# Optimization experiments

Hardware: AMD Instinct MI355X
Metric: run time of the kernel (lower is better)

## Reference

```python
import jax, jax.numpy as jnp
import numpy as np

ANCHOR_SIZES = (128.0, 256.0, 512.0)
ANCHOR_RATIOS = (0.5, 1.0, 2.0)
IOU_THR = 0.3


def _conv(x, w, b, pad):
    y = jax.lax.conv_general_dilated(
        x, w, window_strides=(1, 1), padding=[(pad, pad), (pad, pad)],
        dimension_numbers=("NCHW", "OIHW", "NCHW"))
    return y + b[None, :, None, None]


def _make_anchors(grid_h, grid_w, stride):
    # torchvision-style cell anchors (ratio-major over scales), rounded
    scales = jnp.asarray(ANCHOR_SIZES, jnp.float32)
    ratios = jnp.asarray(ANCHOR_RATIOS, jnp.float32)
    h_r = jnp.sqrt(ratios)
    w_r = 1.0 / h_r
    ws = (w_r[:, None] * scales[None, :]).reshape(-1)  # (A,)
    hs = (h_r[:, None] * scales[None, :]).reshape(-1)
    base = jnp.round(jnp.stack([-ws, -hs, ws, hs], axis=1) / 2.0)  # (A,4)
    sx = jnp.arange(grid_w, dtype=jnp.float32) * stride
    sy = jnp.arange(grid_h, dtype=jnp.float32) * stride
    yy, xx = jnp.meshgrid(sy, sx, indexing="ij")
    shifts = jnp.stack([xx, yy, xx, yy], axis=-1).reshape(-1, 4)  # (HW,4)
    return (shifts[:, None, :] + base[None, :, :]).reshape(-1, 4)  # (HW*A,4)


def _apply_box(anchors, deltas):
    w = anchors[:, 2] - anchors[:, 0]
    h = anchors[:, 3] - anchors[:, 1]
    cx = anchors[:, 0] + 0.5 * w
    cy = anchors[:, 1] + 0.5 * h
    pcx = deltas[:, 0] * w + cx
    pcy = deltas[:, 1] * h + cy
    pw = jnp.exp(deltas[:, 2]) * w
    ph = jnp.exp(deltas[:, 3]) * h
    return jnp.stack([pcx - 0.5 * pw, pcy - 0.5 * ph,
                      pcx + 0.5 * pw, pcy + 0.5 * ph], axis=1)


def _clip(boxes, img_h, img_w):
    x1 = jnp.clip(boxes[:, 0], 0.0, img_w)
    y1 = jnp.clip(boxes[:, 1], 0.0, img_h)
    x2 = jnp.clip(boxes[:, 2], 0.0, img_w)
    y2 = jnp.clip(boxes[:, 3], 0.0, img_h)
    return jnp.stack([x1, y1, x2, y2], axis=1)


def _nms_keep(boxes, scores, thr):
    # returns boolean keep mask in ORIGINAL box order (all idxs identical in
    # the source's batched_nms call, so this is plain NMS)
    n = boxes.shape[0]
    order = jnp.argsort(-scores)
    b = boxes[order]
    area = (b[:, 2] - b[:, 0]) * (b[:, 3] - b[:, 1])
    lt = jnp.maximum(b[:, None, :2], b[None, :, :2])
    rb = jnp.minimum(b[:, None, 2:], b[None, :, 2:])
    wh = jnp.clip(rb - lt, 0.0, None)
    inter = wh[..., 0] * wh[..., 1]
    iou = inter / (area[:, None] + area[None, :] - inter + 1e-9)  # (N,N)
    idx = jnp.arange(n)

    def body(i, keep):
        sup = (iou[i] > thr) & (idx > i)
        return jnp.where(keep[i], keep & ~sup, keep)

    keep_sorted = jax.lax.fori_loop(0, n, body, jnp.ones(n, bool))
    return jnp.zeros(n, bool).at[order].set(keep_sorted)


def setup_inputs() -> dict:
    key = jax.random.key(0)
    ks = jax.random.split(key, 7)
    C, H, W = 256, 32, 32
    A = len(ANCHOR_SIZES) * len(ANCHOR_RATIOS)  # 9
    return {
        "features": jax.random.normal(ks[0], (1, C, H, W), jnp.float32),
        "image_size": 512,
        "conv_w": jax.random.normal(ks[1], (512, C, 3, 3), jnp.float32) * 0.01,
        "conv_b": jnp.zeros((512,), jnp.float32),
        "cls_w": jax.random.normal(ks[2], (2 * A, 512, 1, 1), jnp.float32) * 0.01,
        "cls_b": jnp.zeros((2 * A,), jnp.float32),
        "bbox_w": jax.random.normal(ks[3], (4 * A, 512, 1, 1), jnp.float32) * 0.01,
        "bbox_b": jnp.zeros((4 * A,), jnp.float32),
    }


def reference(features, image_size, conv_w, conv_b, cls_w, cls_b, bbox_w, bbox_b):
    img_h = img_w = float(image_size)
    x = jax.nn.relu(_conv(features, conv_w, conv_b, pad=1))
    logits = _conv(x, cls_w, cls_b, pad=0)          # (1, 2A, H, W)
    bbox_pred = _conv(x, bbox_w, bbox_b, pad=0)     # (1, 4A, H, W)
    probs = jax.nn.sigmoid(logits)
    fg_scores = probs[:, 1::2, :, :].reshape(-1)    # same flatten order as torch
    grid_h, grid_w = features.shape[2], features.shape[3]
    stride = image_size // grid_h
    anchors = _make_anchors(grid_h, grid_w, float(stride))
    proposals = _apply_box(anchors, bbox_pred.reshape(-1, 4))
    proposals = _clip(proposals, img_h, img_w)
    keep = _nms_keep(proposals, fg_scores, IOU_THR)
    # fixed-shape output: suppressed boxes zeroed, plus the keep mask
    return proposals * keep[:, None].astype(proposals.dtype), probs, keep
```

## Files before the change

### kernel.cpp

```cpp
#include <hip/hip_runtime.h>
#include <math.h>

#define X_B      0
#define BBOX_B   2097152
#define PROPS_B  2244608
#define KEYS_B   2392064
#define RANK_B   2465792
#define SKEYS_B  2502656
#define SBOX_B   2576384
#define MASK_B   2725888
#define INTRA_B  KEYS_B
#define WS_NEED  13400000

typedef unsigned long long u64;
typedef double v4d __attribute__((ext_vector_type(4)));

__global__ __launch_bounds__(256, 2) void conv3x3_mfma_k(
    const float* __restrict__ feat, const float* __restrict__ w,
    const float* __restrict__ bias, float* __restrict__ xout)
{
  __shared__ float wl[9216];
  __shared__ float fl[8704];

  const int tid = threadIdx.x;
  const int ct = blockIdx.x >> 4;
  const int g  = blockIdx.x & 15;
  const int co0 = ct << 4;
  const int y0  = g << 1;

  for (int i = tid; i < 8704; i += 256) fl[i] = 0.0f;

  const int lane = tid & 63, wv = tid >> 6;
  const int q = lane >> 4, n = lane & 15;
  const int wy = wv >> 1, xb = (wv & 1) << 4;
  const int xn = xb + n;

  v4d ac0 = {0.0, 0.0, 0.0, 0.0}, ac1 = {0.0, 0.0, 0.0, 0.0};
  v4d ac2 = {0.0, 0.0, 0.0, 0.0}, ac3 = {0.0, 0.0, 0.0, 0.0};
  const float4* feat4 = (const float4*)feat;

  __syncthreads();

  for (int c = 0; c < 4; ++c) {
    const int cb = c << 6;
    #pragma unroll
    for (int i = 0; i < 9; ++i) {
      const int idx4 = tid + (i << 8);
      const int co = idx4 / 144;
      const int s4 = idx4 - co * 144;
      const float4 v =
          *(const float4*)(w + (co0 + co) * 2304 + c * 576 + (s4 << 2));
      #pragma unroll
      for (int e = 0; e < 4; ++e) {
        const int s = (s4 << 2) + e;
        const int ci = s / 9;
        const int tap = s - ci * 9;
        wl[(((tap << 6) + ci) << 4) + co] = ((const float*)&v)[e];
      }
    }
    #pragma unroll
    for (int i = 0; i < 8; ++i) {
      const int idx4 = tid + (i << 8);
      const int ci = idx4 >> 5;
      const int rr = (idx4 >> 3) & 3;
      const int x4 = idx4 & 7;
      const int grow = y0 - 1 + rr;
      if ((unsigned)grow < 32u) {
        const float4 v = feat4[((cb + ci) << 8) + (grow << 3) + x4];
        float* p = &fl[ci * 136 + rr * 34 + 1 + (x4 << 2)];
        p[0] = v.x; p[1] = v.y; p[2] = v.z; p[3] = v.w;
      }
    }
    __syncthreads();
    #pragma unroll
    for (int tap = 0; tap < 9; ++tap) {
      const int ky = tap / 3, kx = tap - 3 * (tap / 3);
      const float* ab = &wl[(tap << 10) + (q << 4) + n];
      const float* bb = &fl[q * 136 + (wy + ky) * 34 + xn + kx];
      #pragma unroll
      for (int u = 0; u < 16; u += 4) {
        ac0 = __builtin_amdgcn_mfma_f64_16x16x4f64(
            (double)ab[(u + 0) << 6], (double)bb[(u + 0) * 544], ac0, 0, 0, 0);
        ac1 = __builtin_amdgcn_mfma_f64_16x16x4f64(
            (double)ab[(u + 1) << 6], (double)bb[(u + 1) * 544], ac1, 0, 0, 0);
        ac2 = __builtin_amdgcn_mfma_f64_16x16x4f64(
            (double)ab[(u + 2) << 6], (double)bb[(u + 2) * 544], ac2, 0, 0, 0);
        ac3 = __builtin_amdgcn_mfma_f64_16x16x4f64(
            (double)ab[(u + 3) << 6], (double)bb[(u + 3) * 544], ac3, 0, 0, 0);
      }
    }
    __syncthreads();
  }

  const int pbase = (g << 6) + (wv << 4) + n;
  #pragma unroll
  for (int i = 0; i < 4; ++i) {
    const int co = co0 + q + (i << 2);
    const double s = (ac0[i] + ac1[i]) + (ac2[i] + ac3[i]);
    const double v = fmax(s + (double)bias[co], 0.0);
    xout[(co << 10) + pbase] = (float)v;
  }
}

#define CPITCH 38
#define CCHS   (18 * CPITCH)
__global__ __launch_bounds__(256) void conv3x3_relu_fb_k(
    const float* __restrict__ feat, const float* __restrict__ w,
    const float* __restrict__ bias, float* __restrict__ xout)
{
  __shared__ float il[2][8 * CCHS];
  const int cp = blockIdx.x >> 1, h = blockIdx.x & 1;
  const int tid = threadIdx.x;
  const int h16 = h << 4;
  const int co0 = cp << 1;
  for (int i = tid; i < 8 * CCHS; i += 256) { il[0][i] = 0.0f; il[1][i] = 0.0f; }
  const int yl = tid >> 4;
  const int x0 = (tid & 15) << 1;
  double aA0 = 0.0, aA1 = 0.0, aB0 = 0.0, aB1 = 0.0;
  const float4* feat4 = (const float4*)feat;
  float4 pf[5]; int pch[5], pt[5], pc4[5], pok[5];
  #pragma unroll
  for (int k = 0; k < 5; ++k) {
    const int i = tid + (k << 8);
    const int ch = i / 144, rem = i - ch * 144;
    const int t = rem >> 3, c4 = rem & 7;
    const int g = h16 - 1 + t;
    pch[k] = ch; pt[k] = t; pc4[k] = c4;
    pok[k] = (i < 1152) && ((unsigned)g < 32u);
    pf[k] = pok[k] ? feat4[(ch << 8) + (g << 3) + c4] : float4{0.f,0.f,0.f,0.f};
  }
  __syncthreads();
  for (int cc = 0; cc < 256; cc += 8) {
    const int buf = (cc >> 3) & 1;
    #pragma unroll
    for (int k = 0; k < 5; ++k)
      if (pok[k]) {
        float* p = &il[buf][pch[k] * CCHS + pt[k] * CPITCH + (pc4[k] << 2) + 1];
        p[0] = pf[k].x; p[1] = pf[k].y; p[2] = pf[k].z; p[3] = pf[k].w;
      }
    if (cc + 8 < 256) {
      #pragma unroll
      for (int k = 0; k < 5; ++k) {
        const int g = h16 - 1 + pt[k];
        if (pok[k]) pf[k] = feat4[((cc + 8 + pch[k]) << 8) + (g << 3) + pc4[k]];
      }
    }
    __syncthreads();
    #pragma unroll
    for (int cl = 0; cl < 8; ++cl) {
      const float* wAp = w + co0 * 2304 + (cc + cl) * 9;
      const float* wBp = wAp + 2304;
      double wa[9], wb[9];
      #pragma unroll
      for (int q = 0; q < 9; ++q) { wa[q] = (double)wAp[q]; wb[q] = (double)wBp[q]; }
      const float* ir = &il[buf][cl * CCHS + yl * CPITCH + x0];
      #pragma unroll
      for (int ky = 0; ky < 3; ++ky) {
        const float2 q0 = *(const float2*)(ir + ky * CPITCH);
        const float2 q1 = *(const float2*)(ir + ky * CPITCH + 2);
        const double v0 = (double)q0.x, v1 = (double)q0.y;
        const double v2 = (double)q1.x, v3 = (double)q1.y;
        aA0 += v0 * wa[3*ky+0] + v1 * wa[3*ky+1] + v2 * wa[3*ky+2];
        aA1 += v1 * wa[3*ky+0] + v2 * wa[3*ky+1] + v3 * wa[3*ky+2];
        aB0 += v0 * wb[3*ky+0] + v1 * wb[3*ky+1] + v2 * wb[3*ky+2];
        aB1 += v1 * wb[3*ky+0] + v2 * wb[3*ky+1] + v3 * wb[3*ky+2];
      }
    }
  }
  const double bA = (double)bias[co0], bB = (double)bias[co0 + 1];
  const int y = h16 + yl;
  float2 rA, rB;
  rA.x = (float)fmax(aA0 + bA, 0.0); rA.y = (float)fmax(aA1 + bA, 0.0);
  rB.x = (float)fmax(aB0 + bB, 0.0); rB.y = (float)fmax(aB1 + bB, 0.0);
  *(float2*)&xout[(co0 << 10) + (y << 5) + x0] = rA;
  *(float2*)&xout[((co0 + 1) << 10) + (y << 5) + x0] = rB;
}

__global__ __launch_bounds__(256) void head1x1_k(
    const float* __restrict__ x,
    const float* __restrict__ cls_w, const float* __restrict__ cls_b,
    const float* __restrict__ bbox_w, const float* __restrict__ bbox_b,
    float* __restrict__ out, float* __restrict__ bbox_out)
{
  __shared__ float wl[512];
  const int bid = blockIdx.x;
  const int co = bid >> 2;
  const int px = ((bid & 3) << 8) | threadIdx.x;
  const bool is_cls = co < 18;
  const float* wsrc = is_cls ? (cls_w + co * 512) : (bbox_w + (co - 18) * 512);
  for (int i = threadIdx.x; i < 512; i += 256) wl[i] = wsrc[i];
  __syncthreads();
  double acc0 = 0.0, acc1 = 0.0, acc2 = 0.0, acc3 = 0.0;
  #pragma unroll 4
  for (int c = 0; c < 512; c += 4) {
    acc0 += (double)x[((c + 0) << 10) | px] * (double)wl[c + 0];
    acc1 += (double)x[((c + 1) << 10) | px] * (double)wl[c + 1];
    acc2 += (double)x[((c + 2) << 10) | px] * (double)wl[c + 2];
    acc3 += (double)x[((c + 3) << 10) | px] * (double)wl[c + 3];
  }
  double acc = ((acc0 + acc1) + (acc2 + acc3)) +
               (double)(is_cls ? cls_b[co] : bbox_b[co - 18]);
  if (is_cls)
    out[36864 + (co << 10) + px] = (float)(1.0 / (1.0 + exp(-acc)));
  else
    bbox_out[((co - 18) << 10) + px] = (float)acc;
}

__global__ __launch_bounds__(256) void proposals_k(
    const float* __restrict__ bbox, const int* __restrict__ imgsz,
    const float* __restrict__ out, float* __restrict__ props,
    u64* __restrict__ keys, unsigned* __restrict__ rank)
{
  const int r = blockIdx.x * 256 + threadIdx.x;
  if (r >= 9216) return;
  const float4 d = ((const float4*)bbox)[r];
  const int cell = r / 9, a = r - cell * 9;
  const int ix = cell & 31, iy = cell >> 5;
  const int ri = a / 3, si = a - ri * 3;
  const double ratio = (ri == 0) ? 0.5 : (ri == 1 ? 1.0 : 2.0);
  const double scale = (si == 0) ? 128.0 : (si == 1 ? 256.0 : 512.0);
  const double hr = sqrt(ratio), wr = 1.0 / hr;
  const double bx = nearbyint(wr * scale * 0.5);
  const double by = nearbyint(hr * scale * 0.5);
  const double cx = ix * 16.0, cy = iy * 16.0;
  const double w = 2.0 * bx, hh = 2.0 * by;
  const double pcx = (double)d.x * w + cx;
  const double pcy = (double)d.y * hh + cy;
  const double pw = exp((double)d.z) * w;
  const double ph = exp((double)d.w) * hh;
  const double im = (double)imgsz[0];
  float4 o;
  o.x = (float)fmin(fmax(pcx - 0.5 * pw, 0.0), im);
  o.y = (float)fmin(fmax(pcy - 0.5 * ph, 0.0), im);
  o.z = (float)fmin(fmax(pcx + 0.5 * pw, 0.0), im);
  o.w = (float)fmin(fmax(pcy + 0.5 * ph, 0.0), im);
  ((float4*)props)[r] = o;
  const float s = out[36864 + ((2 * (r >> 10) + 1) << 10) + (r & 1023)];
  keys[r] = ((u64)__float_as_uint(s) << 32) | (unsigned)(0x7FFFFFFF - r);
  rank[r] = 0u;
}

__global__ __launch_bounds__(256) void rank_k(
    const u64* __restrict__ keys, unsigned* __restrict__ rank)
{
  const int jt = blockIdx.x % 36, ic = blockIdx.x / 36;
  const int j = jt * 256 + threadIdx.x;
  const u64 kj = keys[j];
  const int lane = threadIdx.x & 63;
  const int base = ic * 576;
  unsigned lo[9], hi[9];
  #pragma unroll
  for (int rr = 0; rr < 9; ++rr) {
    const u64 k = keys[base + rr * 64 + lane];
    lo[rr] = (unsigned)k; hi[rr] = (unsigned)(k >> 32);
  }
  unsigned cnt = 0;
  #pragma unroll
  for (int rr = 0; rr < 9; ++rr) {
    #pragma unroll
    for (int l = 0; l < 64; ++l) {
      const unsigned llo = (unsigned)__builtin_amdgcn_readlane((int)lo[rr], l);
      const unsigned lhi = (unsigned)__builtin_amdgcn_readlane((int)hi[rr], l);
      const u64 ki = ((u64)lhi << 32) | llo;
      cnt += (ki > kj) ? 1u : 0u;
    }
  }
  atomicAdd(&rank[j], cnt);
}

__global__ __launch_bounds__(256) void scatter_k(
    const u64* __restrict__ keys, const unsigned* __restrict__ rank,
    const float* __restrict__ props, u64* __restrict__ skeys,
    float4* __restrict__ sboxes)
{
  const int r = blockIdx.x * 256 + threadIdx.x;
  if (r >= 9216) return;
  const unsigned rk = rank[r];
  skeys[rk] = keys[r];
  sboxes[rk] = ((const float4*)props)[r];
}

__global__ __launch_bounds__(256) void mask_k(
    const float4* __restrict__ sb4, u64* __restrict__ mask,
    u64* __restrict__ intra)
{
  __shared__ __align__(16) float4 ib[64];
  const int ci = blockIdx.x;
  const int Wb = blockIdx.y << 2;
  const int i_lo = ci << 6;
  const int i_hi = min(i_lo + 64, (Wb + 4) << 6);
  if (i_lo >= i_hi) return;
  const int wv = threadIdx.x >> 6, lane = threadIdx.x & 63;
  const int W = Wb + wv;
  const int cnt = i_hi - i_lo;
  if (threadIdx.x < cnt) ib[threadIdx.x] = sb4[i_lo + threadIdx.x];
  __syncthreads();
  const float4 bj = sb4[(W << 6) + lane];
  const float areaJ = (bj.z - bj.x) * (bj.w - bj.y);
  const int wbase = W << 6;
  const int n = min(i_hi, wbase + 64) - i_lo;
  u64 intr = 0ULL;
  #pragma unroll 8
  for (int k = 0; k < n; ++k) {
    const float4 bi = ib[k];
    const float areaI = (bi.z - bi.x) * (bi.w - bi.y);
    const float ix1 = fmaxf(bj.x, bi.x), iy1 = fmaxf(bj.y, bi.y);
    const float ix2 = fminf(bj.z, bi.z), iy2 = fminf(bj.w, bi.w);
    const float iw = fmaxf(ix2 - ix1, 0.0f), ih = fmaxf(iy2 - iy1, 0.0f);
    const double inter = (double)iw * (double)ih;
    const double uni = (double)areaJ + (double)areaI - inter + 1e-9;
    const bool pred = inter > 0.3 * uni;
    const u64 bal = __ballot(pred);
    const int i = i_lo + k;
    if (lane == 0) mask[(size_t)i * 144 + W] = bal;
    if (i >= wbase) intr |= pred ? (1ULL << (i - wbase)) : 0ULL;
  }
  if (ci == W) intra[wbase + lane] = intr;
}

__global__ __launch_bounds__(1024) void sweep_out_k(
    const u64* __restrict__ mask, const u64* __restrict__ intra,
    const u64* __restrict__ skeys, const float4* __restrict__ sboxes,
    float* __restrict__ out)
{
  extern __shared__ __align__(16) char sm[];
  u64* subm   = (u64*)sm;
  u64* intraS = subm + 8192;
  u64* supS   = intraS + 1024;
  u64* keptS  = supS + 16;
  unsigned short* kpl = (unsigned short*)(keptS + 144);
  int* kcnt = (int*)(kpl + 9216);

  const int tid = threadIdx.x;
  const int lane = tid & 63, wv = tid >> 6;
  if (tid == 0) *kcnt = 0;
  if (tid < 144) keptS[tid] = 0ULL;
  if (tid < 16) supS[tid] = 0ULL;
  if (tid < 512) {
    const int wq = tid & 7, r0 = tid >> 3;
    #pragma unroll
    for (int k = 0; k < 8; ++k) {
      const int i = r0 + (k << 6);
      subm[i * 8 + wq] = mask[(size_t)i * 144 + wq];
    }
    if (wq == 0) intraS[r0] = intra[r0];
    if (wq == 1) intraS[64 + r0] = intra[64 + r0];
    if (wq == 2) intraS[128 + r0] = intra[128 + r0];
    if (wq == 3) intraS[192 + r0] = intra[192 + r0];
    if (wq == 4) intraS[256 + r0] = intra[256 + r0];
    if (wq == 5) intraS[320 + r0] = intra[320 + r0];
    if (wq == 6) intraS[384 + r0] = intra[384 + r0];
    if (wq == 7) intraS[448 + r0] = intra[448 + r0];
  }
  __syncthreads();

  for (int sg = 0; sg < 18; ++sg) {
    const int buf = sg & 1;
    const int wbase = sg << 3;
    const int ibase = wbase << 6;
    if (tid < 512) {
      const int K = *kcnt;
      const int wq = tid & 7;
      u64 acc = 0ULL;
      int jj = tid >> 3;
      for (; jj + 7 * 64 < K; jj += 8 * 64) {
        const u64 v0 = mask[(size_t)kpl[jj + 0 * 64] * 144 + wbase + wq];
        const u64 v1 = mask[(size_t)kpl[jj + 1 * 64] * 144 + wbase + wq];
        const u64 v2 = mask[(size_t)kpl[jj + 2 * 64] * 144 + wbase + wq];
        const u64 v3 = mask[(size_t)kpl[jj + 3 * 64] * 144 + wbase + wq];
        const u64 v4 = mask[(size_t)kpl[jj + 4 * 64] * 144 + wbase + wq];
        const u64 v5 = mask[(size_t)kpl[jj + 5 * 64] * 144 + wbase + wq];
        const u64 v6 = mask[(size_t)kpl[jj + 6 * 64] * 144 + wbase + wq];
        const u64 v7 = mask[(size_t)kpl[jj + 7 * 64] * 144 + wbase + wq];
        acc |= ((v0 | v1) | (v2 | v3)) | ((v4 | v5) | (v6 | v7));
      }
      for (; jj < K; jj += 64)
        acc |= mask[(size_t)kpl[jj] * 144 + wbase + wq];
      if (acc) {
        atomicOr((unsigned*)&supS[(buf << 3) + wq], (unsigned)acc);
        atomicOr(((unsigned*)&supS[(buf << 3) + wq]) + 1, (unsigned)(acc >> 32));
      }
    }
    __syncthreads();
    if (wv == 0) {
      u64 myAlive = (lane < 8) ? ~supS[(buf << 3) + lane] : 0ULL;
      const u64* sub = subm + (buf << 12);
      const u64* its = intraS + (buf << 9);
      for (int w = 0; w < 8; ++w) {
        const u64 av = __shfl(myAlive, w, 64);
        if (av == 0ULL) continue;
        const u64 il_ = its[(w << 6) + lane];
        u64 cand = av, keptw = 0ULL;
        while (cand) {
          const int b = (int)__builtin_ctzll(cand);
          keptw |= 1ULL << b;
          cand &= ~(1ULL << b);
          const u64 sup = __ballot((il_ >> b) & 1ULL);
          cand &= ~sup;
        }
        if (lane == 0) {
          keptS[wbase + w] = keptw;
          int K = *kcnt;
          u64 t = keptw;
          while (t) {
            const int b = (int)__builtin_ctzll(t); t &= t - 1ULL;
            kpl[K++] = (unsigned short)(ibase + (w << 6) + b);
          }
          *kcnt = K;
        }
        u64 t = keptw;
        while (t) {
          int bs[8]; int n = 0;
          #pragma unroll
          for (int s = 0; s < 8; ++s) {
            if (t) { bs[s] = (int)__builtin_ctzll(t); t &= t - 1ULL; n = s + 1; }
            else bs[s] = 0;
          }
          const int kk = lane >> 3, wq = lane & 7;
          u64 r = (kk < n) ? sub[((w << 6) + bs[kk]) * 8 + wq] : 0ULL;
          r |= __shfl_down(r, 8, 64);
          r |= __shfl_down(r, 16, 64);
          r |= __shfl_down(r, 32, 64);
          myAlive &= ~r;
        }
      }
    } else if (wv == 1) {
      if (lane < 8) supS[((1 - buf) << 3) + lane] = 0ULL;
    } else if (wv >= 8 && sg + 1 < 18) {
      const int s = tid - 512;
      const int wq = s & 7, r0 = s >> 3;
      const int nb = 1 - buf;
      const int ib2 = (sg + 1) << 9;
      const int wb2 = (sg + 1) << 3;
      #pragma unroll
      for (int k = 0; k < 8; ++k) {
        const int i = r0 + (k << 6);
        subm[(nb << 12) + i * 8 + wq] = mask[(size_t)(ib2 + i) * 144 + wb2 + wq];
      }
      if (wq < 8) {
        const int idx = (wq << 6) + r0;
        intraS[(nb << 9) + idx] = intra[ib2 + idx];
      }
    }
    __syncthreads();
  }
  for (int i = tid; i < 9216; i += 1024) {
    const u64 key = skeys[i];
    const int orig = 0x7FFFFFFF - (int)(unsigned)(key & 0xFFFFFFFFULL);
    const bool kp = (keptS[i >> 6] >> (i & 63)) & 1ULL;
    float4 ob = sboxes[i];
    if (!kp) { ob.x = 0.f; ob.y = 0.f; ob.z = 0.f; ob.w = 0.f; }
    ((float4*)out)[orig] = ob;
    out[55296 + orig] = kp ? 1.0f : 0.0f;
  }
}

__global__ __launch_bounds__(1024) void nms_fallback_k(
    const float* __restrict__ props, float* __restrict__ out)
{
  __shared__ u64 wmax[16];
  __shared__ float4 curBoxS;
  const int tid = threadIdx.x, wid = tid >> 6, lane = tid & 63;
  u64 key[9];
  float4 box[9];
  #pragma unroll
  for (int j = 0; j < 9; ++j) {
    const int r = tid + (j << 10);
    box[j] = ((const float4*)props)[r];
    const float s = out[36864 + ((2 * (r >> 10) + 1) << 10) + (r & 1023)];
    key[j] = ((u64)__float_as_uint(s) << 32) | (unsigned)(0x7FFFFFFF - r);
  }
  unsigned kept = 0;
  for (;;) {
    u64 m = key[0];
    #pragma unroll
    for (int j = 1; j < 9; ++j) m = key[j] > m ? key[j] : m;
    #pragma unroll
    for (int off = 32; off; off >>= 1) {
      const u64 o = __shfl_down(m, off, 64);
      if (o > m) m = o;
    }
    if (lane == 0) wmax[wid] = m;
    __syncthreads();
    u64 K = wmax[0];
    #pragma unroll
    for (int wv2 = 1; wv2 < 16; ++wv2) { const u64 t = wmax[wv2]; if (t > K) K = t; }
    if (K == 0) break;
    #pragma unroll
    for (int j = 0; j < 9; ++j)
      if (key[j] == K) { curBoxS = box[j]; key[j] = 0; kept |= 1u << j; }
    __syncthreads();
    const float4 cb = curBoxS;
    const float areaC = (cb.z - cb.x) * (cb.w - cb.y);
    #pragma unroll
    for (int j = 0; j < 9; ++j) {
      if (key[j]) {
        const float4 b = box[j];
        const float ix1 = fmaxf(b.x, cb.x), iy1 = fmaxf(b.y, cb.y);
        const float ix2 = fminf(b.z, cb.z), iy2 = fminf(b.w, cb.w);
        const float iw = fmaxf(ix2 - ix1, 0.0f), ih = fmaxf(iy2 - iy1, 0.0f);
        const float areaB = (b.z - b.x) * (b.w - b.y);
        const double inter = (double)iw * (double)ih;
        const double uni = (double)areaB + (double)areaC - inter + 1e-9;
        if (inter > 0.3 * uni) key[j] = 0;
      }
    }
    __syncthreads();
  }
  #pragma unroll
  for (int j = 0; j < 9; ++j) {
    const int r = tid + (j << 10);
    const bool kp = (kept >> j) & 1u;
    float4 ob = box[j];
    if (!kp) { ob.x = 0.f; ob.y = 0.f; ob.z = 0.f; ob.w = 0.f; }
    ((float4*)out)[r] = ob;
    out[55296 + r] = kp ? 1.0f : 0.0f;
  }
}

extern "C" void kernel_launch(void* const* d_in, const int* in_sizes, int n_in,
                              void* d_out, int out_size, void* d_ws, size_t ws_size,
                              hipStream_t stream)
{
  const float* feat   = (const float*)d_in[0];
  const int*   imgsz  = (const int*)d_in[1];
  const float* conv_w = (const float*)d_in[2];
  const float* conv_b = (const float*)d_in[3];
  const float* cls_w  = (const float*)d_in[4];
  const float* cls_b  = (const float*)d_in[5];
  const float* bbox_w = (const float*)d_in[6];
  const float* bbox_b = (const float*)d_in[7];
  float* out = (float*)d_out;
  char*  ws  = (char*)d_ws;
  float* x      = (float*)(ws + X_B);
  float* bbox   = (float*)(ws + BBOX_B);
  float* props  = (float*)(ws + PROPS_B);
  u64*      keys  = (u64*)(ws + KEYS_B);
  unsigned* rankp = (unsigned*)(ws + RANK_B);
  u64*      skeys = (u64*)(ws + SKEYS_B);
  float4*   sboxs = (float4*)(ws + SBOX_B);
  u64*      maskp = (u64*)(ws + MASK_B);
  u64*      intrp = (u64*)(ws + INTRA_B);

  if (ws_size >= (size_t)WS_NEED) {
    hipLaunchKernelGGL(conv3x3_mfma_k, dim3(512), dim3(256), 0, stream,
                       feat, conv_w, conv_b, x);
    hipLaunchKernelGGL(head1x1_k, dim3(216), dim3(256), 0, stream,
                       x, cls_w, cls_b, bbox_w, bbox_b, out, bbox);
    hipLaunchKernelGGL(proposals_k, dim3(36), dim3(256), 0, stream,
                       bbox, imgsz, out, props, keys, rankp);
    hipLaunchKernelGGL(rank_k, dim3(576), dim3(256), 0, stream, keys, rankp);
    hipLaunchKernelGGL(scatter_k, dim3(36), dim3(256), 0, stream,
                       keys, rankp, props, skeys, sboxs);
    hipLaunchKernelGGL(mask_k, dim3(144, 36), dim3(256), 0, stream,
                       sboxs, maskp, intrp);
    hipLaunchKernelGGL(sweep_out_k, dim3(1), dim3(1024), 93444, stream,
                       maskp, intrp, skeys, sboxs, out);
  } else {
    hipLaunchKernelGGL(conv3x3_relu_fb_k, dim3(512), dim3(256), 0, stream,
                       feat, conv_w, conv_b, x);
    hipLaunchKernelGGL(head1x1_k, dim3(216), dim3(256), 0, stream,
                       x, cls_w, cls_b, bbox_w, bbox_b, out, bbox);
    hipLaunchKernelGGL(proposals_k, dim3(36), dim3(256), 0, stream,
                       bbox, imgsz, out, props, keys, rankp);
    hipLaunchKernelGGL(nms_fallback_k, dim3(1), dim3(1024), 0, stream,
                       props, out);
  }
}
```

Baseline: 281.8 us.

## Make NMS sweep incremental over new keepers and drop separate intra-word mask

The single-block sweep no longer re-ORs suppression rows from every kept box for each 512-box group. It keeps a running suppression vector for all 144 words and, per group, folds in only the rows of keepers added since the previous group, spread across all 1024 threads. The separate intra-word mask buffer is removed: the diagonal word is read from the padded shared submatrix (stride 9) and broadcast with readlane instead of ballot. Keeper list appends are done in parallel with popcount prefixes. The serial NMS critical path should shrink, at the cost of 64-bit shared atomics and a more complex indexing scheme.

```diff
diff --git a/kernel.cpp b/kernel.cpp
--- a/kernel.cpp
+++ b/kernel.cpp
@@ -9,7 +9,6 @@
 #define SKEYS_B  2502656
 #define SBOX_B   2576384
 #define MASK_B   2725888
-#define INTRA_B  KEYS_B
 #define WS_NEED  13400000
 
 typedef unsigned long long u64;
@@ -281,8 +280,7 @@
 }
 
 __global__ __launch_bounds__(256) void mask_k(
-    const float4* __restrict__ sb4, u64* __restrict__ mask,
-    u64* __restrict__ intra)
+    const float4* __restrict__ sb4, u64* __restrict__ mask)
 {
   __shared__ __align__(16) float4 ib[64];
   const int ci = blockIdx.x;
@@ -297,9 +295,7 @@
   __syncthreads();
   const float4 bj = sb4[(W << 6) + lane];
   const float areaJ = (bj.z - bj.x) * (bj.w - bj.y);
-  const int wbase = W << 6;
-  const int n = min(i_hi, wbase + 64) - i_lo;
-  u64 intr = 0ULL;
+  const int n = i_hi - i_lo;
   #pragma unroll 8
   for (int k = 0; k < n; ++k) {
     const float4 bi = ib[k];
@@ -313,44 +309,32 @@
     const u64 bal = __ballot(pred);
     const int i = i_lo + k;
     if (lane == 0) mask[(size_t)i * 144 + W] = bal;
-    if (i >= wbase) intr |= pred ? (1ULL << (i - wbase)) : 0ULL;
-  }
-  if (ci == W) intra[wbase + lane] = intr;
+  }
 }
 
 __global__ __launch_bounds__(1024) void sweep_out_k(
-    const u64* __restrict__ mask, const u64* __restrict__ intra,
-    const u64* __restrict__ skeys, const float4* __restrict__ sboxes,
-    float* __restrict__ out)
+    const u64* __restrict__ mask, const u64* __restrict__ skeys,
+    const float4* __restrict__ sboxes, float* __restrict__ out)
 {
   extern __shared__ __align__(16) char sm[];
   u64* subm   = (u64*)sm;
-  u64* intraS = subm + 8192;
-  u64* supS   = intraS + 1024;
-  u64* keptS  = supS + 16;
+  u64* supAll = subm + 9216;
+  u64* keptS  = supAll + 144;
   unsigned short* kpl = (unsigned short*)(keptS + 144);
-  int* kcnt = (int*)(kpl + 9216);
+  int* kcnt  = (int*)(kpl + 9216);
+  int* kprev = kcnt + 1;
 
   const int tid = threadIdx.x;
   const int lane = tid & 63, wv = tid >> 6;
-  if (tid == 0) *kcnt = 0;
-  if (tid < 144) keptS[tid] = 0ULL;
-  if (tid < 16) supS[tid] = 0ULL;
+  if (tid == 0) { *kcnt = 0; *kprev = 0; }
+  if (tid < 144) { keptS[tid] = 0ULL; supAll[tid] = 0ULL; }
   if (tid < 512) {
     const int wq = tid & 7, r0 = tid >> 3;
     #pragma unroll
     for (int k = 0; k < 8; ++k) {
       const int i = r0 + (k << 6);
-      subm[i * 8 + wq] = mask[(size_t)i * 144 + wq];
-    }
-    if (wq == 0) intraS[r0] = intra[r0];
-    if (wq == 1) intraS[64 + r0] = intra[64 + r0];
-    if (wq == 2) intraS[128 + r0] = intra[128 + r0];
-    if (wq == 3) intraS[192 + r0] = intra[192 + r0];
-    if (wq == 4) intraS[256 + r0] = intra[256 + r0];
-    if (wq == 5) intraS[320 + r0] = intra[320 + r0];
-    if (wq == 6) intraS[384 + r0] = intra[384 + r0];
-    if (wq == 7) intraS[448 + r0] = intra[448 + r0];
+      subm[i * 9 + wq] = mask[(size_t)i * 144 + wq];
+    }
   }
   __syncthreads();
 
@@ -358,74 +342,64 @@
     const int buf = sg & 1;
     const int wbase = sg << 3;
     const int ibase = wbase << 6;
-    if (tid < 512) {
-      const int K = *kcnt;
-      const int wq = tid & 7;
-      u64 acc = 0ULL;
-      int jj = tid >> 3;
-      for (; jj + 7 * 64 < K; jj += 8 * 64) {
-        const u64 v0 = mask[(size_t)kpl[jj + 0 * 64] * 144 + wbase + wq];
-        const u64 v1 = mask[(size_t)kpl[jj + 1 * 64] * 144 + wbase + wq];
-        const u64 v2 = mask[(size_t)kpl[jj + 2 * 64] * 144 + wbase + wq];
-        const u64 v3 = mask[(size_t)kpl[jj + 3 * 64] * 144 + wbase + wq];
-        const u64 v4 = mask[(size_t)kpl[jj + 4 * 64] * 144 + wbase + wq];
-        const u64 v5 = mask[(size_t)kpl[jj + 5 * 64] * 144 + wbase + wq];
-        const u64 v6 = mask[(size_t)kpl[jj + 6 * 64] * 144 + wbase + wq];
-        const u64 v7 = mask[(size_t)kpl[jj + 7 * 64] * 144 + wbase + wq];
-        acc |= ((v0 | v1) | (v2 | v3)) | ((v4 | v5) | (v6 | v7));
-      }
-      for (; jj < K; jj += 64)
-        acc |= mask[(size_t)kpl[jj] * 144 + wbase + wq];
-      if (acc) {
-        atomicOr((unsigned*)&supS[(buf << 3) + wq], (unsigned)acc);
-        atomicOr(((unsigned*)&supS[(buf << 3) + wq]) + 1, (unsigned)(acc >> 32));
+    const int P = *kprev, K = *kcnt;
+    if (K > P) {
+      const int nW = 144 - wbase;
+      const int S = 1024 / nW;
+      const int wi = tid % nW, sl = tid / nW;
+      if (sl < S) {
+        u64 acc = 0ULL;
+        for (int j = P + sl; j < K; j += S)
+          acc |= mask[(size_t)kpl[j] * 144 + wbase + wi];
+        if (acc) atomicOr(&supAll[wbase + wi], acc);
       }
     }
     __syncthreads();
     if (wv == 0) {
-      u64 myAlive = (lane < 8) ? ~supS[(buf << 3) + lane] : 0ULL;
-      const u64* sub = subm + (buf << 12);
-      const u64* its = intraS + (buf << 9);
+      u64 myAlive = (lane < 8) ? ~supAll[wbase + lane] : 0ULL;
+      const u64* sub = subm + buf * 4608;
       for (int w = 0; w < 8; ++w) {
         const u64 av = __shfl(myAlive, w, 64);
         if (av == 0ULL) continue;
-        const u64 il_ = its[(w << 6) + lane];
+        const u64 rowL = sub[((w << 6) + lane) * 9 + w];
         u64 cand = av, keptw = 0ULL;
         while (cand) {
           const int b = (int)__builtin_ctzll(cand);
           keptw |= 1ULL << b;
-          cand &= ~(1ULL << b);
-          const u64 sup = __ballot((il_ >> b) & 1ULL);
-          cand &= ~sup;
+          const u64 sup =
+              ((u64)(unsigned)__builtin_amdgcn_readlane((int)(rowL >> 32), b)
+               << 32) |
+              (unsigned)__builtin_amdgcn_readlane((int)rowL, b);
+          cand &= ~(sup | (1ULL << b));
         }
-        if (lane == 0) {
-          keptS[wbase + w] = keptw;
-          int K = *kcnt;
+        if (lane == 0) keptS[wbase + w] = keptw;
+        if (keptw) {
+          const int K2 = *kcnt;
+          if ((keptw >> lane) & 1ULL) {
+            const int pre =
+                __builtin_popcountll(keptw & ((1ULL << lane) - 1ULL));
+            kpl[K2 + pre] = (unsigned short)(ibase + (w << 6) + lane);
+          }
+          if (lane == 0) *kcnt = K2 + __builtin_popcountll(keptw);
           u64 t = keptw;
           while (t) {
-            const int b = (int)__builtin_ctzll(t); t &= t - 1ULL;
-            kpl[K++] = (unsigned short)(ibase + (w << 6) + b);
+            int bs[8]; int nn = 0;
+            #pragma unroll
+            for (int s = 0; s < 8; ++s) {
+              if (t) { bs[s] = (int)__builtin_ctzll(t); t &= t - 1ULL; nn = s + 1; }
+              else bs[s] = 0;
+            }
+            const int kk = lane >> 3, wq = lane & 7;
+            u64 r = (kk < nn) ? sub[((w << 6) + bs[kk]) * 9 + wq] : 0ULL;
+            r |= __shfl_down(r, 8, 64);
+            r |= __shfl_down(r, 16, 64);
+            r |= __shfl_down(r, 32, 64);
+            myAlive &= ~r;
           }
-          *kcnt = K;
         }
-        u64 t = keptw;
-        while (t) {
-          int bs[8]; int n = 0;
-          #pragma unroll
-          for (int s = 0; s < 8; ++s) {
-            if (t) { bs[s] = (int)__builtin_ctzll(t); t &= t - 1ULL; n = s + 1; }
-            else bs[s] = 0;
-          }
-          const int kk = lane >> 3, wq = lane & 7;
-          u64 r = (kk < n) ? sub[((w << 6) + bs[kk]) * 8 + wq] : 0ULL;
-          r |= __shfl_down(r, 8, 64);
-          r |= __shfl_down(r, 16, 64);
-          r |= __shfl_down(r, 32, 64);
-          myAlive &= ~r;
-        }
       }
     } else if (wv == 1) {
-      if (lane < 8) supS[((1 - buf) << 3) + lane] = 0ULL;
+      if (lane == 0) *kprev = K;
     } else if (wv >= 8 && sg + 1 < 18) {
       const int s = tid - 512;
       const int wq = s & 7, r0 = s >> 3;
@@ -435,11 +409,7 @@
       #pragma unroll
       for (int k = 0; k < 8; ++k) {
         const int i = r0 + (k << 6);
-        subm[(nb << 12) + i * 8 + wq] = mask[(size_t)(ib2 + i) * 144 + wb2 + wq];
-      }
-      if (wq < 8) {
-        const int idx = (wq << 6) + r0;
-        intraS[(nb << 9) + idx] = intra[ib2 + idx];
+        subm[nb * 4608 + i * 9 + wq] = mask[(size_t)(ib2 + i) * 144 + wb2 + wq];
       }
     }
     __syncthreads();
@@ -540,7 +510,6 @@
   u64*      skeys = (u64*)(ws + SKEYS_B);
   float4*   sboxs = (float4*)(ws + SBOX_B);
   u64*      maskp = (u64*)(ws + MASK_B);
-  u64*      intrp = (u64*)(ws + INTRA_B);
 
   if (ws_size >= (size_t)WS_NEED) {
     hipLaunchKernelGGL(conv3x3_mfma_k, dim3(512), dim3(256), 0, stream,
@@ -553,9 +522,9 @@
     hipLaunchKernelGGL(scatter_k, dim3(36), dim3(256), 0, stream,
                        keys, rankp, props, skeys, sboxs);
     hipLaunchKernelGGL(mask_k, dim3(144, 36), dim3(256), 0, stream,
-                       sboxs, maskp, intrp);
-    hipLaunchKernelGGL(sweep_out_k, dim3(1), dim3(1024), 93444, stream,
-                       maskp, intrp, skeys, sboxs, out);
+                       sboxs, maskp);
+    hipLaunchKernelGGL(sweep_out_k, dim3(1), dim3(1024), 94472, stream,
+                       maskp, skeys, sboxs, out);
   } else {
     hipLaunchKernelGGL(conv3x3_relu_fb_k, dim3(512), dim3(256), 0, stream,
                        feat, conv_w, conv_b, x);
```

Result: faster. 272.7 us (-3.2%).
